# Optimization experiments

Measured on AMD Instinct MI355X. Metric: run time of the kernel, lower is better.

Reference implementation:

```python
import jax, jax.numpy as jnp
import numpy as np

N, E, F, R, S = 20000, 320000, 64, 8, 10
AVG_NEIGH = 16.0


def setup_inputs() -> dict:
    key = jax.random.key(0)
    ks = jax.random.split(key, 16)
    inp = {
        "vectors": jax.random.normal(ks[0], (E, 3), jnp.float32),
        "node_feats": jax.random.normal(ks[1], (N, F, 4), jnp.float32),  # [N, F, 1(0e)+3(1o)]
        "node_specie": jax.random.randint(ks[2], (N,), 0, S),
        "radial_embedding": jax.random.normal(ks[3], (E, R), jnp.float32),
        "senders": jax.random.randint(ks[4], (E,), 0, N),
        "receivers": jax.random.randint(ks[5], (E,), 0, N),
        # residual FullyConnectedTensorProduct(feats, one-hot species 0e) == species-dep. linear per l
        "W_res_s": jax.random.normal(ks[6], (S, F, F), jnp.float32),
        "W_res_v": jax.random.normal(ks[7], (S, F, F), jnp.float32),
        # interaction block: input linear per l
        "W_in_s": jax.random.normal(ks[8], (F, F), jnp.float32),
        "W_in_v": jax.random.normal(ks[9], (F, F), jnp.float32),
        # radial MLP -> 5 CG tensor-product path weights per channel
        "mlp_w1": jax.random.normal(ks[10], (R, 64), jnp.float32),
        "mlp_w2": jax.random.normal(ks[11], (64, 5 * F), jnp.float32) / 8.0,
        # interaction block: output linear per l
        "W_out_s": jax.random.normal(ks[12], (F, F), jnp.float32),
        "W_out_v": jax.random.normal(ks[13], (F, F), jnp.float32),
        # symmetric product basis (correlation 3), species-dependent term weights
        "W_prod_s": jax.random.normal(ks[14], (S, 5, F), jnp.float32) * 0.3,
        "W_prod_v": jax.random.normal(ks[15], (S, 4, F), jnp.float32) * 0.3,
    }
    k2 = jax.random.split(jax.random.key(1), 3)
    inp["W_lin_s"] = jax.random.normal(k2[0], (F, F), jnp.float32)
    inp["W_lin_v"] = jax.random.normal(k2[1], (F, F), jnp.float32)
    inp["W_read"] = jax.random.normal(k2[2], (F, 1), jnp.float32)
    return inp


def _forward(vectors, node_feats, node_specie, radial_embedding, senders, receivers,
             W_res_s, W_res_v, W_in_s, W_in_v, mlp_w1, mlp_w2, W_out_s, W_out_v,
             W_prod_s, W_prod_v, W_lin_s, W_lin_v, W_read):
    inv_sf = 1.0 / jnp.sqrt(jnp.float32(F))
    s = node_feats[..., 0]          # [N,F]   0e channels
    v = node_feats[..., 1:]         # [N,F,3] 1o channels

    # --- residual connection: FCTP(feats, one-hot species 0e attrs) -> species-gated linear per l
    res_s = jnp.einsum('nf,ngf->ng', s, W_res_s[node_specie]) * inv_sf
    res_v = jnp.einsum('nfc,ngf->ngc', v, W_res_v[node_specie]) * inv_sf

    # --- InteractionBlock ---
    h_s = (s @ W_in_s) * inv_sf
    h_v = jnp.einsum('nfc,fg->ngc', v, W_in_v) * inv_sf

    # spherical harmonics up to max_ell=1: Y0 = 1, Y1 = unit edge vector
    r = jnp.sqrt(jnp.sum(vectors * vectors, -1) + 1e-12)
    Y1 = vectors / r[:, None]                                # [E,3]

    # radial MLP produces per-edge weights for the 5 CG paths:
    # (0e x Y0 -> 0e), (1o . Y1 -> 0e), (0e x Y1 -> 1o), (1o x Y0 -> 1o), (1o x Y1 -> 1o, cross)
    w = (jax.nn.silu(radial_embedding @ mlp_w1) @ mlp_w2).reshape(-1, 5, F)  # [E,5,F]

    ss = h_s[senders]                                        # [E,F]
    sv = h_v[senders]                                        # [E,F,3]
    dot = jnp.einsum('efc,ec->ef', sv, Y1)                   # [E,F]
    m_s = w[:, 0] * ss + w[:, 1] * dot                       # [E,F]
    m_v = (w[:, 2] * ss)[:, :, None] * Y1[:, None, :] \
        + w[:, 3][:, :, None] * sv \
        + w[:, 4][:, :, None] * jnp.cross(sv, Y1[:, None, :])  # [E,F,3]

    agg_s = jnp.zeros_like(h_s).at[receivers].add(m_s) / AVG_NEIGH
    agg_v = jnp.zeros_like(h_v).at[receivers].add(m_v) / AVG_NEIGH
    a_s = (agg_s @ W_out_s) * inv_sf
    a_v = jnp.einsum('nfc,fg->ngc', agg_v, W_out_v) * inv_sf

    # --- EquivariantProductBasisBlock: correlation-3 symmetric contraction, species-dependent ---
    vv = jnp.sum(a_v * a_v, -1)                              # [N,F] invariant |v|^2
    Wp = W_prod_s[node_specie]                               # [N,5,F]
    p_s = (Wp[:, 0] * a_s + Wp[:, 1] * a_s ** 2 + Wp[:, 2] * a_s ** 3
           + Wp[:, 3] * vv + Wp[:, 4] * a_s * vv)
    Wv = W_prod_v[node_specie]                               # [N,4,F]
    p_v = (Wv[:, 0] + Wv[:, 1] * a_s + Wv[:, 2] * a_s ** 2 + Wv[:, 3] * vv)[:, :, None] * a_v

    f_s = (p_s @ W_lin_s) * inv_sf + res_s
    f_v = jnp.einsum('nfc,fg->ngc', p_v, W_lin_v) * inv_sf + res_v

    # --- LinearReadoutBlock (output_irreps = 0e), 1 head ---
    node_out = ((f_s @ W_read) * inv_sf)[:, None, :]         # [N, heads=1, 1]
    new_feats = jnp.concatenate([f_s[..., None], f_v], axis=-1)  # [N,F,4]
    return node_out, new_feats


def reference(vectors, node_feats, node_specie, radial_embedding, senders, receivers,
              W_res_s, W_res_v, W_in_s, W_in_v, mlp_w1, mlp_w2, W_out_s, W_out_v,
              W_prod_s, W_prod_v, W_lin_s, W_lin_v, W_read):
    return _forward(vectors, node_feats, node_specie, radial_embedding, senders, receivers,
                    W_res_s, W_res_v, W_in_s, W_in_v, mlp_w1, mlp_w2, W_out_s, W_out_v,
                    W_prod_s, W_prod_v, W_lin_s, W_lin_v, W_read)
```

## Files before the change

kernel.cpp:

```cpp
#include <hip/hip_runtime.h>
#include <math.h>

#define NN 20000
#define NE 320000
#define NF (NN*64)

typedef short sh8_t  __attribute__((ext_vector_type(8)));
typedef float fl4_t  __attribute__((ext_vector_type(4)));

__device__ __forceinline__ float silu_f(float x){ return x / (1.0f + expf(-x)); }

__device__ __forceinline__ short f2bf(float f){
  unsigned u = __builtin_bit_cast(unsigned, f);
  unsigned r = (u + 0x7fffu + ((u >> 16) & 1u)) >> 16;
  return (short)r;
}
__device__ __forceinline__ float bf2f(short s){
  unsigned u = ((unsigned)(unsigned short)s) << 16;
  return __builtin_bit_cast(float, u);
}

__global__ __launch_bounds__(256) void k_prep_w2(
    const float* __restrict__ w2, short* __restrict__ w2f)
{
  int i = blockIdx.x*256 + threadIdx.x;
  int jp   = i & 7;
  int lane = (i >> 3) & 63;
  int frag = i >> 9;
  int k2 = frag / 20, p = frag % 20;
  int j = p >> 2, T = p & 3;
  int k = k2*32 + (lane >> 4)*8 + jp;
  int n = j*64 + T*16 + (lane & 15);
  w2f[i] = f2bf(w2[k*320 + n]);
}

__global__ __launch_bounds__(256) void k_transpose_res(
    const float* __restrict__ Ws, const float* __restrict__ Wv,
    float* __restrict__ Wst, float* __restrict__ Wvt)
{
  int i = blockIdx.x*256 + threadIdx.x;
  int spec = i >> 12;
  int g = (i >> 6) & 63;
  int f = i & 63;
  Wst[spec*4096 + f*64 + g] = Ws[i];
  Wvt[spec*4096 + f*64 + g] = Wv[i];
}

__global__ __launch_bounds__(256) void k_node_pre(
    const float* __restrict__ node_feats, const float* __restrict__ W_in_s,
    const float* __restrict__ W_in_v, float* __restrict__ h_s, float* __restrict__ h_v)
{
  __shared__ float4 sh[4][8][64];
  int wave = threadIdx.x >> 6, lane = threadIdx.x & 63;
  int n0 = blockIdx.x*32 + wave*8;
  #pragma unroll
  for(int nd=0; nd<8; ++nd)
    sh[wave][nd][lane] = *(const float4*)(node_feats + ((size_t)(n0+nd)*64 + lane)*4);
  float as[8], av0[8], av1[8], av2[8];
  #pragma unroll
  for(int nd=0; nd<8; ++nd){ as[nd]=0.f; av0[nd]=0.f; av1[nd]=0.f; av2[nd]=0.f; }
  for(int f=0; f<64; ++f){
    float ws = W_in_s[f*64+lane], wv = W_in_v[f*64+lane];
    #pragma unroll
    for(int nd=0; nd<8; ++nd){
      float4 t = sh[wave][nd][f];
      as[nd]  += t.x*ws;
      av0[nd] += t.y*wv;
      av1[nd] += t.z*wv;
      av2[nd] += t.w*wv;
    }
  }
  #pragma unroll
  for(int nd=0; nd<8; ++nd){
    int o = (n0+nd)*64 + lane;
    h_s[o]      = as[nd] *0.125f;
    h_v[o]      = av0[nd]*0.125f;
    h_v[NF+o]   = av1[nd]*0.125f;
    h_v[2*NF+o] = av2[nd]*0.125f;
  }
}

__global__ __launch_bounds__(256) void k_edge(
    const float* __restrict__ vectors, const float* __restrict__ radial,
    const int* __restrict__ senders, const int* __restrict__ receivers,
    const float* __restrict__ mlp_w1, const short* __restrict__ w2f,
    const float* __restrict__ h_s, const float* __restrict__ h_v,
    float* __restrict__ agg_s, float* __restrict__ agg_v)
{
  __shared__ float hid[4][16][68];
  __shared__ float ey[4][16][3];
  __shared__ int   esr[4][16][2];
  __shared__ float rad[4][128];
  int wave = threadIdx.x >> 6, lane = threadIdx.x & 63;
  int e0 = blockIdx.x*64 + wave*16;

  rad[wave][lane]    = radial[e0*8 + lane];
  rad[wave][64+lane] = radial[e0*8 + 64 + lane];
  if(lane < 16){
    int e = e0 + lane;
    float vx = vectors[3*e], vy = vectors[3*e+1], vz = vectors[3*e+2];
    float rinv = 1.0f/sqrtf(vx*vx + vy*vy + vz*vz + 1e-12f);
    ey[wave][lane][0]=vx*rinv; ey[wave][lane][1]=vy*rinv; ey[wave][lane][2]=vz*rinv;
    esr[wave][lane][0]=senders[e]; esr[wave][lane][1]=receivers[e];
  }
  float w1r[8];
  #pragma unroll
  for(int r=0; r<8; ++r) w1r[r] = mlp_w1[r*64+lane];
  #pragma unroll
  for(int t=0; t<16; ++t){
    float acc = 0.f;
    #pragma unroll
    for(int r=0; r<8; ++r) acc += rad[wave][t*8+r]*w1r[r];
    hid[wave][t][lane] = silu_f(acc);
  }

  fl4_t C[20];
  #pragma unroll
  for(int p=0; p<20; ++p) C[p] = (fl4_t){0.f,0.f,0.f,0.f};
  int l15 = lane & 15, q = lane >> 4;
  #pragma unroll
  for(int k2=0; k2<2; ++k2){
    const float* hp = &hid[wave][l15][k2*32 + q*8];
    float a[8];
    #pragma unroll
    for(int i=0; i<8; ++i) a[i] = hp[i];
    sh8_t ahi, alo;
    #pragma unroll
    for(int i=0; i<8; ++i){
      short h = f2bf(a[i]);
      ahi[i] = h;
      alo[i] = f2bf(a[i] - bf2f(h));
    }
    const short* bbase = w2f + (size_t)(k2*20)*512 + lane*8;
    #pragma unroll
    for(int p=0; p<20; ++p){
      sh8_t b = *(const sh8_t*)(bbase + p*512);
      C[p] = __builtin_amdgcn_mfma_f32_16x16x32_bf16(ahi, b, C[p], 0, 0, 0);
      C[p] = __builtin_amdgcn_mfma_f32_16x16x32_bf16(alo, b, C[p], 0, 0, 0);
    }
  }

  #pragma unroll
  for(int reg=0; reg<4; ++reg){
    int r = q*4 + reg;
    float y0 = ey[wave][r][0], y1 = ey[wave][r][1], y2 = ey[wave][r][2];
    int snd = esr[wave][r][0], rcv = esr[wave][r][1];
    #pragma unroll
    for(int T=0; T<4; ++T){
      int c = T*16 + l15;
      int so = snd*64 + c, ro = rcv*64 + c;
      float ss  = h_s[so];
      float sv0 = h_v[so], sv1 = h_v[NF+so], sv2 = h_v[2*NF+so];
      float dot = sv0*y0 + sv1*y1 + sv2*y2;
      float w0 = C[T][reg], w1v = C[4+T][reg], w2v = C[8+T][reg];
      float w3v = C[12+T][reg], w4v = C[16+T][reg];
      float ms  = w0*ss + w1v*dot;
      float w2s = w2v*ss;
      float mv0 = w2s*y0 + w3v*sv0 + w4v*(sv1*y2 - sv2*y1);
      float mv1 = w2s*y1 + w3v*sv1 + w4v*(sv2*y0 - sv0*y2);
      float mv2 = w2s*y2 + w3v*sv2 + w4v*(sv0*y1 - sv1*y0);
      atomicAdd(&agg_s[ro],      ms);
      atomicAdd(&agg_v[ro],      mv0);
      atomicAdd(&agg_v[NF+ro],   mv1);
      atomicAdd(&agg_v[2*NF+ro], mv2);
    }
  }
}

__global__ __launch_bounds__(256) void k_node_post(
  const float* __restrict__ node_feats, const int* __restrict__ specie,
  const float* __restrict__ agg_s, const float* __restrict__ agg_v,
  const float* __restrict__ Wrst, const float* __restrict__ Wrvt,
  const float* __restrict__ W_out_s, const float* __restrict__ W_out_v,
  const float* __restrict__ W_prod_s, const float* __restrict__ W_prod_v,
  const float* __restrict__ W_lin_s, const float* __restrict__ W_lin_v,
  const float* __restrict__ W_read, float* __restrict__ out_node, float* __restrict__ out_feats)
{
  __shared__ float4 buf[4][8][64];
  int wave = threadIdx.x >> 6, lane = threadIdx.x & 63;
  int n0 = blockIdx.x*32 + wave*8;
  int sp[8];
  #pragma unroll
  for(int nd=0; nd<8; ++nd) sp[nd] = specie[n0+nd];

  #pragma unroll
  for(int nd=0; nd<8; ++nd){
    int o = (n0+nd)*64 + lane;
    buf[wave][nd][lane] = make_float4(agg_s[o]*(1.f/16.f), agg_v[o]*(1.f/16.f),
                                      agg_v[NF+o]*(1.f/16.f), agg_v[2*NF+o]*(1.f/16.f));
  }
  float a_s[8], a0[8], a1[8], a2[8];
  #pragma unroll
  for(int nd=0; nd<8; ++nd){ a_s[nd]=0.f; a0[nd]=0.f; a1[nd]=0.f; a2[nd]=0.f; }
  for(int f=0; f<64; ++f){
    float wos = W_out_s[f*64+lane], wov = W_out_v[f*64+lane];
    #pragma unroll
    for(int nd=0; nd<8; ++nd){
      float4 t = buf[wave][nd][f];
      a_s[nd] += t.x*wos; a0[nd] += t.y*wov; a1[nd] += t.z*wov; a2[nd] += t.w*wov;
    }
  }
  #pragma unroll
  for(int nd=0; nd<8; ++nd){ a_s[nd]*=0.125f; a0[nd]*=0.125f; a1[nd]*=0.125f; a2[nd]*=0.125f; }

  #pragma unroll
  for(int nd=0; nd<8; ++nd)
    buf[wave][nd][lane] = *(const float4*)(node_feats + ((size_t)(n0+nd)*64 + lane)*4);
  float r_s[8], r0[8], r1[8], r2[8];
  #pragma unroll
  for(int nd=0; nd<8; ++nd){ r_s[nd]=0.f; r0[nd]=0.f; r1[nd]=0.f; r2[nd]=0.f; }
  for(int f=0; f<64; ++f){
    #pragma unroll
    for(int nd=0; nd<8; ++nd){
      float wrs = Wrst[sp[nd]*4096 + f*64 + lane];
      float wrv = Wrvt[sp[nd]*4096 + f*64 + lane];
      float4 t = buf[wave][nd][f];
      r_s[nd] += t.x*wrs; r0[nd] += t.y*wrv; r1[nd] += t.z*wrv; r2[nd] += t.w*wrv;
    }
  }
  #pragma unroll
  for(int nd=0; nd<8; ++nd){ r_s[nd]*=0.125f; r0[nd]*=0.125f; r1[nd]*=0.125f; r2[nd]*=0.125f; }

  #pragma unroll
  for(int nd=0; nd<8; ++nd){
    float vv = a0[nd]*a0[nd] + a1[nd]*a1[nd] + a2[nd]*a2[nd];
    float as2 = a_s[nd]*a_s[nd];
    const float* Wp = W_prod_s + sp[nd]*320;
    float p_s = Wp[lane]*a_s[nd] + Wp[64+lane]*as2 + Wp[128+lane]*as2*a_s[nd]
              + Wp[192+lane]*vv + Wp[256+lane]*a_s[nd]*vv;
    const float* Wq = W_prod_v + sp[nd]*256;
    float coef = Wq[lane] + Wq[64+lane]*a_s[nd] + Wq[128+lane]*as2 + Wq[192+lane]*vv;
    buf[wave][nd][lane] = make_float4(p_s, coef*a0[nd], coef*a1[nd], coef*a2[nd]);
  }
  float fs[8], f0[8], f1[8], f2[8];
  #pragma unroll
  for(int nd=0; nd<8; ++nd){ fs[nd]=0.f; f0[nd]=0.f; f1[nd]=0.f; f2[nd]=0.f; }
  for(int f=0; f<64; ++f){
    float wls = W_lin_s[f*64+lane], wlv = W_lin_v[f*64+lane];
    #pragma unroll
    for(int nd=0; nd<8; ++nd){
      float4 t = buf[wave][nd][f];
      fs[nd] += t.x*wls; f0[nd] += t.y*wlv; f1[nd] += t.z*wlv; f2[nd] += t.w*wlv;
    }
  }
  float wr = W_read[lane];
  #pragma unroll
  for(int nd=0; nd<8; ++nd){
    float vs = fs[nd]*0.125f + r_s[nd];
    float v0 = f0[nd]*0.125f + r0[nd];
    float v1 = f1[nd]*0.125f + r1[nd];
    float v2 = f2[nd]*0.125f + r2[nd];
    int o = (n0+nd)*64 + lane;
    float4 o4; o4.x=vs; o4.y=v0; o4.z=v1; o4.w=v2;
    *(float4*)(out_feats + (size_t)o*4) = o4;
    float x = vs * wr;
    #pragma unroll
    for(int off=32; off; off>>=1) x += __shfl_down(x, off);
    if(lane==0) out_node[n0+nd] = x*0.125f;
  }
}

extern "C" void kernel_launch(void* const* d_in, const int* in_sizes, int n_in,
                              void* d_out, int out_size, void* d_ws, size_t ws_size,
                              hipStream_t stream) {
  const float* vectors    = (const float*)d_in[0];
  const float* node_feats = (const float*)d_in[1];
  const int*   node_specie= (const int*)  d_in[2];
  const float* radial     = (const float*)d_in[3];
  const int*   senders    = (const int*)  d_in[4];
  const int*   receivers  = (const int*)  d_in[5];
  const float* W_res_s    = (const float*)d_in[6];
  const float* W_res_v    = (const float*)d_in[7];
  const float* W_in_s     = (const float*)d_in[8];
  const float* W_in_v     = (const float*)d_in[9];
  const float* mlp_w1     = (const float*)d_in[10];
  const float* mlp_w2     = (const float*)d_in[11];
  const float* W_out_s    = (const float*)d_in[12];
  const float* W_out_v    = (const float*)d_in[13];
  const float* W_prod_s   = (const float*)d_in[14];
  const float* W_prod_v   = (const float*)d_in[15];
  const float* W_lin_s    = (const float*)d_in[16];
  const float* W_lin_v    = (const float*)d_in[17];
  const float* W_read     = (const float*)d_in[18];

  float* ws   = (float*)d_ws;
  float* h_s  = ws;
  float* h_v  = ws + NF;
  float* agg_s= ws + 4*(size_t)NF;
  float* agg_v= ws + 5*(size_t)NF;
  float* Wrst = ws + 8*(size_t)NF;
  float* Wrvt = ws + 8*(size_t)NF + 40960;
  short* w2f  = (short*)(ws + 8*(size_t)NF + 81920);

  hipMemsetAsync(agg_s, 0, (size_t)4*NF*sizeof(float), stream);
  k_prep_w2<<<80, 256, 0, stream>>>(mlp_w2, w2f);
  k_transpose_res<<<160, 256, 0, stream>>>(W_res_s, W_res_v, Wrst, Wrvt);
  k_node_pre<<<625, 256, 0, stream>>>(node_feats, W_in_s, W_in_v, h_s, h_v);
  k_edge<<<NE/64, 256, 0, stream>>>(vectors, radial, senders, receivers,
                                    mlp_w1, w2f, h_s, h_v, agg_s, agg_v);
  k_node_post<<<625, 256, 0, stream>>>(node_feats, node_specie, agg_s, agg_v,
                                       Wrst, Wrvt, W_out_s, W_out_v,
                                       W_prod_s, W_prod_v, W_lin_s, W_lin_v,
                                       W_read, (float*)d_out, (float*)d_out + NN);
}
```

Baseline: 541.7 us.

## Replace atomic edge scatter with receiver-sorted CSR gather aggregation

Each call now builds a receiver-sorted CSR index with a histogram, a single-block scan and an atomic scatter. The edge kernel becomes one wave per receiver node: it walks that node's edges in chunks of 16, accumulates messages in registers, reduces across lanes with shuffles, and writes each output once. This removes the float atomics to agg_s/agg_v and the memset of the aggregate buffers. The cost is padded MFMA work on partial chunks, load imbalance across nodes of different degree, and the extra index-building kernels. The residual linear in k_node_post is also reordered to loop over nodes first, then features.

```diff
diff --git a/kernel.cpp b/kernel.cpp
--- a/kernel.cpp
+++ b/kernel.cpp
@@ -18,6 +18,47 @@
 __device__ __forceinline__ float bf2f(short s){
   unsigned u = ((unsigned)(unsigned short)s) << 16;
   return __builtin_bit_cast(float, u);
+}
+
+__global__ __launch_bounds__(256) void k_hist(
+    const int* __restrict__ receivers, int* __restrict__ counts)
+{
+  int i = blockIdx.x*256 + threadIdx.x;
+  atomicAdd(&counts[receivers[i]], 1);
+}
+
+__global__ __launch_bounds__(256) void k_scan(
+    const int* __restrict__ counts, int* __restrict__ row_start, int* __restrict__ off2)
+{
+  __shared__ int part[256];
+  __shared__ int excl[257];
+  int t = threadIdx.x;
+  int lo = t*79, hi = lo+79 < NN ? lo+79 : NN;
+  int s = 0;
+  for(int i=lo; i<hi; ++i) s += counts[i];
+  part[t] = s;
+  __syncthreads();
+  if(t == 0){
+    int a = 0;
+    for(int i=0; i<256; ++i){ excl[i] = a; a += part[i]; }
+    excl[256] = a;
+  }
+  __syncthreads();
+  int a = excl[t];
+  for(int i=lo; i<hi; ++i){
+    int c = counts[i];
+    row_start[i] = a; off2[i] = a;
+    a += c;
+  }
+  if(t == 255) row_start[NN] = excl[256];
+}
+
+__global__ __launch_bounds__(256) void k_scatter(
+    const int* __restrict__ receivers, int* __restrict__ off2, int* __restrict__ csr)
+{
+  int e = blockIdx.x*256 + threadIdx.x;
+  int pos = atomicAdd(&off2[receivers[e]], 1);
+  csr[pos] = e;
 }
 
 __global__ __launch_bounds__(256) void k_prep_w2(
@@ -80,91 +121,123 @@
   }
 }
 
-__global__ __launch_bounds__(256) void k_edge(
+__global__ __launch_bounds__(256) void k_edge_recv(
     const float* __restrict__ vectors, const float* __restrict__ radial,
-    const int* __restrict__ senders, const int* __restrict__ receivers,
+    const int* __restrict__ senders,
+    const int* __restrict__ row_start, const int* __restrict__ csr,
     const float* __restrict__ mlp_w1, const short* __restrict__ w2f,
     const float* __restrict__ h_s, const float* __restrict__ h_v,
     float* __restrict__ agg_s, float* __restrict__ agg_v)
 {
   __shared__ float hid[4][16][68];
   __shared__ float ey[4][16][3];
-  __shared__ int   esr[4][16][2];
+  __shared__ int   esn[4][16];
   __shared__ float rad[4][128];
   int wave = threadIdx.x >> 6, lane = threadIdx.x & 63;
-  int e0 = blockIdx.x*64 + wave*16;
-
-  rad[wave][lane]    = radial[e0*8 + lane];
-  rad[wave][64+lane] = radial[e0*8 + 64 + lane];
-  if(lane < 16){
-    int e = e0 + lane;
-    float vx = vectors[3*e], vy = vectors[3*e+1], vz = vectors[3*e+2];
-    float rinv = 1.0f/sqrtf(vx*vx + vy*vy + vz*vz + 1e-12f);
-    ey[wave][lane][0]=vx*rinv; ey[wave][lane][1]=vy*rinv; ey[wave][lane][2]=vz*rinv;
-    esr[wave][lane][0]=senders[e]; esr[wave][lane][1]=receivers[e];
-  }
+  int n = blockIdx.x*4 + wave;
+  int start = row_start[n], end = row_start[n+1];
+  int l15 = lane & 15, q = lane >> 4;
+
   float w1r[8];
   #pragma unroll
   for(int r=0; r<8; ++r) w1r[r] = mlp_w1[r*64+lane];
-  #pragma unroll
-  for(int t=0; t<16; ++t){
-    float acc = 0.f;
-    #pragma unroll
-    for(int r=0; r<8; ++r) acc += rad[wave][t*8+r]*w1r[r];
-    hid[wave][t][lane] = silu_f(acc);
-  }
-
-  fl4_t C[20];
-  #pragma unroll
-  for(int p=0; p<20; ++p) C[p] = (fl4_t){0.f,0.f,0.f,0.f};
-  int l15 = lane & 15, q = lane >> 4;
-  #pragma unroll
-  for(int k2=0; k2<2; ++k2){
-    const float* hp = &hid[wave][l15][k2*32 + q*8];
-    float a[8];
-    #pragma unroll
-    for(int i=0; i<8; ++i) a[i] = hp[i];
-    sh8_t ahi, alo;
-    #pragma unroll
-    for(int i=0; i<8; ++i){
-      short h = f2bf(a[i]);
-      ahi[i] = h;
-      alo[i] = f2bf(a[i] - bf2f(h));
-    }
-    const short* bbase = w2f + (size_t)(k2*20)*512 + lane*8;
-    #pragma unroll
-    for(int p=0; p<20; ++p){
-      sh8_t b = *(const sh8_t*)(bbase + p*512);
-      C[p] = __builtin_amdgcn_mfma_f32_16x16x32_bf16(ahi, b, C[p], 0, 0, 0);
-      C[p] = __builtin_amdgcn_mfma_f32_16x16x32_bf16(alo, b, C[p], 0, 0, 0);
-    }
-  }
-
-  #pragma unroll
-  for(int reg=0; reg<4; ++reg){
-    int r = q*4 + reg;
-    float y0 = ey[wave][r][0], y1 = ey[wave][r][1], y2 = ey[wave][r][2];
-    int snd = esr[wave][r][0], rcv = esr[wave][r][1];
-    #pragma unroll
-    for(int T=0; T<4; ++T){
-      int c = T*16 + l15;
-      int so = snd*64 + c, ro = rcv*64 + c;
-      float ss  = h_s[so];
-      float sv0 = h_v[so], sv1 = h_v[NF+so], sv2 = h_v[2*NF+so];
-      float dot = sv0*y0 + sv1*y1 + sv2*y2;
-      float w0 = C[T][reg], w1v = C[4+T][reg], w2v = C[8+T][reg];
-      float w3v = C[12+T][reg], w4v = C[16+T][reg];
-      float ms  = w0*ss + w1v*dot;
-      float w2s = w2v*ss;
-      float mv0 = w2s*y0 + w3v*sv0 + w4v*(sv1*y2 - sv2*y1);
-      float mv1 = w2s*y1 + w3v*sv1 + w4v*(sv2*y0 - sv0*y2);
-      float mv2 = w2s*y2 + w3v*sv2 + w4v*(sv0*y1 - sv1*y0);
-      atomicAdd(&agg_s[ro],      ms);
-      atomicAdd(&agg_v[ro],      mv0);
-      atomicAdd(&agg_v[NF+ro],   mv1);
-      atomicAdd(&agg_v[2*NF+ro], mv2);
-    }
-  }
+
+  float accS[4]  = {0.f,0.f,0.f,0.f};
+  float accV0[4] = {0.f,0.f,0.f,0.f};
+  float accV1[4] = {0.f,0.f,0.f,0.f};
+  float accV2[4] = {0.f,0.f,0.f,0.f};
+
+  for(int base = start; base < end; base += 16){
+    int rem = end - base;
+    int cnt = rem < 16 ? rem : 16;
+    if(lane < 16){
+      if(lane < cnt){
+        int e = csr[base + lane];
+        float4 r0 = *(const float4*)(radial + (size_t)e*8);
+        float4 r1 = *(const float4*)(radial + (size_t)e*8 + 4);
+        *(float4*)&rad[wave][lane*8]     = r0;
+        *(float4*)&rad[wave][lane*8 + 4] = r1;
+        float vx = vectors[3*e], vy = vectors[3*e+1], vz = vectors[3*e+2];
+        float rinv = 1.0f/sqrtf(vx*vx + vy*vy + vz*vz + 1e-12f);
+        ey[wave][lane][0] = vx*rinv; ey[wave][lane][1] = vy*rinv; ey[wave][lane][2] = vz*rinv;
+        esn[wave][lane] = senders[e];
+      } else {
+        *(float4*)&rad[wave][lane*8]     = (float4){0.f,0.f,0.f,0.f};
+        *(float4*)&rad[wave][lane*8 + 4] = (float4){0.f,0.f,0.f,0.f};
+        ey[wave][lane][0]=0.f; ey[wave][lane][1]=0.f; ey[wave][lane][2]=0.f;
+        esn[wave][lane] = 0;
+      }
+    }
+    #pragma unroll
+    for(int t=0; t<16; ++t){
+      float acc = 0.f;
+      #pragma unroll
+      for(int r=0; r<8; ++r) acc += rad[wave][t*8+r]*w1r[r];
+      hid[wave][t][lane] = silu_f(acc);
+    }
+    fl4_t C[20];
+    #pragma unroll
+    for(int p=0; p<20; ++p) C[p] = (fl4_t){0.f,0.f,0.f,0.f};
+    #pragma unroll
+    for(int k2=0; k2<2; ++k2){
+      const float* hp = &hid[wave][l15][k2*32 + q*8];
+      sh8_t ahi, alo;
+      #pragma unroll
+      for(int i=0; i<8; ++i){
+        float a = hp[i];
+        short h = f2bf(a);
+        ahi[i] = h;
+        alo[i] = f2bf(a - bf2f(h));
+      }
+      const short* bbase = w2f + (size_t)(k2*20)*512 + lane*8;
+      #pragma unroll
+      for(int p=0; p<20; ++p){
+        sh8_t b = *(const sh8_t*)(bbase + p*512);
+        C[p] = __builtin_amdgcn_mfma_f32_16x16x32_bf16(ahi, b, C[p], 0, 0, 0);
+        C[p] = __builtin_amdgcn_mfma_f32_16x16x32_bf16(alo, b, C[p], 0, 0, 0);
+      }
+    }
+    #pragma unroll
+    for(int reg=0; reg<4; ++reg){
+      int r = q*4 + reg;
+      if(r < cnt){
+        float y0 = ey[wave][r][0], y1 = ey[wave][r][1], y2 = ey[wave][r][2];
+        int snd = esn[wave][r];
+        #pragma unroll
+        for(int T=0; T<4; ++T){
+          int c = T*16 + l15;
+          int so = snd*64 + c;
+          float ss  = h_s[so];
+          float sv0 = h_v[so], sv1 = h_v[NF+so], sv2 = h_v[2*NF+so];
+          float dot = sv0*y0 + sv1*y1 + sv2*y2;
+          float w0 = C[T][reg], w1v = C[4+T][reg], w2v = C[8+T][reg];
+          float w3v = C[12+T][reg], w4v = C[16+T][reg];
+          float ms  = w0*ss + w1v*dot;
+          float w2s = w2v*ss;
+          accS[T]  += ms;
+          accV0[T] += w2s*y0 + w3v*sv0 + w4v*(sv1*y2 - sv2*y1);
+          accV1[T] += w2s*y1 + w3v*sv1 + w4v*(sv2*y0 - sv0*y2);
+          accV2[T] += w2s*y2 + w3v*sv2 + w4v*(sv0*y1 - sv1*y0);
+        }
+      }
+    }
+  }
+  #pragma unroll
+  for(int T=0; T<4; ++T){
+    accS[T]  += __shfl_xor(accS[T], 16);  accS[T]  += __shfl_xor(accS[T], 32);
+    accV0[T] += __shfl_xor(accV0[T],16);  accV0[T] += __shfl_xor(accV0[T],32);
+    accV1[T] += __shfl_xor(accV1[T],16);  accV1[T] += __shfl_xor(accV1[T],32);
+    accV2[T] += __shfl_xor(accV2[T],16);  accV2[T] += __shfl_xor(accV2[T],32);
+  }
+  float oS  = (q&2) ? ((q&1)?accS[3] :accS[2])  : ((q&1)?accS[1] :accS[0]);
+  float oV0 = (q&2) ? ((q&1)?accV0[3]:accV0[2]) : ((q&1)?accV0[1]:accV0[0]);
+  float oV1 = (q&2) ? ((q&1)?accV1[3]:accV1[2]) : ((q&1)?accV1[1]:accV1[0]);
+  float oV2 = (q&2) ? ((q&1)?accV2[3]:accV2[2]) : ((q&1)?accV2[1]:accV2[0]);
+  int o = n*64 + lane;
+  agg_s[o]      = oS;
+  agg_v[o]      = oV0;
+  agg_v[NF+o]   = oV1;
+  agg_v[2*NF+o] = oV2;
 }
 
 __global__ __launch_bounds__(256) void k_node_post(
@@ -207,19 +280,17 @@
   for(int nd=0; nd<8; ++nd)
     buf[wave][nd][lane] = *(const float4*)(node_feats + ((size_t)(n0+nd)*64 + lane)*4);
   float r_s[8], r0[8], r1[8], r2[8];
-  #pragma unroll
-  for(int nd=0; nd<8; ++nd){ r_s[nd]=0.f; r0[nd]=0.f; r1[nd]=0.f; r2[nd]=0.f; }
-  for(int f=0; f<64; ++f){
-    #pragma unroll
-    for(int nd=0; nd<8; ++nd){
-      float wrs = Wrst[sp[nd]*4096 + f*64 + lane];
-      float wrv = Wrvt[sp[nd]*4096 + f*64 + lane];
+  for(int nd=0; nd<8; ++nd){
+    const float* Ws_ = Wrst + sp[nd]*4096;
+    const float* Wv_ = Wrvt + sp[nd]*4096;
+    float rs=0.f, rv0=0.f, rv1=0.f, rv2=0.f;
+    for(int f=0; f<64; ++f){
+      float wrs = Ws_[f*64+lane], wrv = Wv_[f*64+lane];
       float4 t = buf[wave][nd][f];
-      r_s[nd] += t.x*wrs; r0[nd] += t.y*wrv; r1[nd] += t.z*wrv; r2[nd] += t.w*wrv;
-    }
-  }
-  #pragma unroll
-  for(int nd=0; nd<8; ++nd){ r_s[nd]*=0.125f; r0[nd]*=0.125f; r1[nd]*=0.125f; r2[nd]*=0.125f; }
+      rs += t.x*wrs; rv0 += t.y*wrv; rv1 += t.z*wrv; rv2 += t.w*wrv;
+    }
+    r_s[nd]=rs*0.125f; r0[nd]=rv0*0.125f; r1[nd]=rv1*0.125f; r2[nd]=rv2*0.125f;
+  }
 
   #pragma unroll
   for(int nd=0; nd<8; ++nd){
@@ -283,21 +354,28 @@
   const float* W_lin_v    = (const float*)d_in[17];
   const float* W_read     = (const float*)d_in[18];
 
-  float* ws   = (float*)d_ws;
-  float* h_s  = ws;
-  float* h_v  = ws + NF;
-  float* agg_s= ws + 4*(size_t)NF;
-  float* agg_v= ws + 5*(size_t)NF;
-  float* Wrst = ws + 8*(size_t)NF;
-  float* Wrvt = ws + 8*(size_t)NF + 40960;
-  short* w2f  = (short*)(ws + 8*(size_t)NF + 81920);
-
-  hipMemsetAsync(agg_s, 0, (size_t)4*NF*sizeof(float), stream);
+  float* ws    = (float*)d_ws;
+  float* h_s   = ws;
+  float* h_v   = ws + NF;
+  float* agg_s = ws + 4*(size_t)NF;
+  float* agg_v = ws + 5*(size_t)NF;
+  float* Wrst  = ws + 8*(size_t)NF;
+  float* Wrvt  = ws + 8*(size_t)NF + 40960;
+  short* w2f   = (short*)(ws + 8*(size_t)NF + 81920);
+  int*   ibase = (int*)(ws + 8*(size_t)NF + 81920 + 10240);
+  int*   row_start = ibase;
+  int*   off2      = ibase + (NN+1);
+  int*   csr       = ibase + (NN+1) + NN;
+
+  hipMemsetAsync(off2, 0, (size_t)NN*sizeof(int), stream);
+  k_hist<<<NE/256, 256, 0, stream>>>(receivers, off2);
+  k_scan<<<1, 256, 0, stream>>>(off2, row_start, off2);
+  k_scatter<<<NE/256, 256, 0, stream>>>(receivers, off2, csr);
   k_prep_w2<<<80, 256, 0, stream>>>(mlp_w2, w2f);
   k_transpose_res<<<160, 256, 0, stream>>>(W_res_s, W_res_v, Wrst, Wrvt);
   k_node_pre<<<625, 256, 0, stream>>>(node_feats, W_in_s, W_in_v, h_s, h_v);
-  k_edge<<<NE/64, 256, 0, stream>>>(vectors, radial, senders, receivers,
-                                    mlp_w1, w2f, h_s, h_v, agg_s, agg_v);
+  k_edge_recv<<<NN/4, 256, 0, stream>>>(vectors, radial, senders, row_start, csr,
+                                        mlp_w1, w2f, h_s, h_v, agg_s, agg_v);
   k_node_post<<<625, 256, 0, stream>>>(node_feats, node_specie, agg_s, agg_v,
                                        Wrst, Wrvt, W_out_s, W_out_v,
                                        W_prod_s, W_prod_v, W_lin_s, W_lin_v,
```

Result: slower. 1.892 ms (+249.3%).
